# Kernel optimization log

Hardware: AMD Instinct MI355X
Metric: run time of the kernel (lower is better)

The kernel has to match this reference:

```python
import jax, jax.numpy as jnp
import numpy as np

B, S, DIN, DOUT = 4, 2048, 4096, 4096
W_SCALE = 64.0   # makes round(weight*scale) produce non-trivial int8 values
X_SCALE = 16.0   # input_scale so x*scale truncates to non-zero int32 values


def setup_inputs() -> dict:
    key = jax.random.key(0)
    k1, k2, k3 = jax.random.split(key, 3)
    # kaiming_uniform fan_in: bound = sqrt(6/fan_in)
    bound = float(np.sqrt(6.0 / DIN))
    weight = jax.random.uniform(k1, (DOUT, DIN), jnp.float32, -bound, bound)
    x = jax.random.normal(k2, (B, S, DIN), jnp.float32)
    bias = jax.random.normal(k3, (DOUT,), jnp.float32) * 0.01
    weight_scale = jnp.full((DOUT,), W_SCALE, jnp.float32)
    input_scale = jnp.full((1,), X_SCALE, jnp.float32)
    return {"x": x, "weight": weight, "bias": bias,
            "weight_scale": weight_scale, "input_scale": input_scale}


def reference(x, weight, bias, weight_scale, input_scale):
    # x = x * input_scale (pre-scale path of forward)
    xs = x * input_scale
    # fake-quant weights: round to int8 with wraparound, like torch .to(int8)
    w_int = jnp.round(weight * weight_scale[:, None]).astype(jnp.int8)
    # x.to(torch.int32): truncation toward zero
    x_int = xs.astype(jnp.int32)
    # F.linear on the integer-valued tensors (computed in f32: values are exact ints)
    acc = jnp.einsum('bsd,od->bso', x_int.astype(jnp.float32),
                     w_int.astype(jnp.float32))
    acc = acc + bias  # bias added inside linear
    # dequant: divide by per-channel weight_scale and the scalar input_scale
    out = acc / (weight_scale * input_scale)
    return out
```

## Files before the change

kernel.cpp:

```cpp
#include <hip/hip_runtime.h>

#define GM 8192
#define GN 4096
#define GK 4096

#define BM 256
#define BN 256
#define BK 64
#define NTILE (GK / BK)
#define ABYTES (BM * BK)
#define TILE_LDS (BM * BK + BN * BK)

using int4v = __attribute__((ext_vector_type(4))) int;

__global__ __launch_bounds__(256) void quant_xw_k(
    const float4* __restrict__ x, unsigned int* __restrict__ xq,
    const float4* __restrict__ w, unsigned int* __restrict__ wq,
    const float* __restrict__ wscale, const float* __restrict__ iscale,
    int n4x, int n4tot) {
    const float xs = *iscale;
    const int stride = gridDim.x * blockDim.x;
    for (int i = blockIdx.x * blockDim.x + threadIdx.x; i < n4tot; i += stride) {
        if (i < n4x) {
            float4 v = x[i];
            int q0 = (int)(v.x * xs);
            int q1 = (int)(v.y * xs);
            int q2 = (int)(v.z * xs);
            int q3 = (int)(v.w * xs);
            xq[i] = (unsigned int)(q0 & 0xff)
                  | ((unsigned int)(q1 & 0xff) << 8)
                  | ((unsigned int)(q2 & 0xff) << 16)
                  | ((unsigned int)(q3 & 0xff) << 24);
        } else {
            int j = i - n4x;
            float s = wscale[j >> 10];
            float4 v = w[j];
            int q0 = (int)rintf(v.x * s);
            int q1 = (int)rintf(v.y * s);
            int q2 = (int)rintf(v.z * s);
            int q3 = (int)rintf(v.w * s);
            wq[j] = (unsigned int)(q0 & 0xff)
                  | ((unsigned int)(q1 & 0xff) << 8)
                  | ((unsigned int)(q2 & 0xff) << 16)
                  | ((unsigned int)(q3 & 0xff) << 24);
        }
    }
}

__global__ __launch_bounds__(512, 2) void qlinear_gemm_i8(
    const signed char* __restrict__ Aq,
    const signed char* __restrict__ Bq,
    const float* __restrict__ bias,
    const float* __restrict__ wscale,
    const float* __restrict__ iscale,
    float* __restrict__ C) {
    __shared__ signed char smem[3 * TILE_LDS];

    const int tid  = threadIdx.x;
    const int wave = tid >> 6;
    const int lane = tid & 63;
    const int m0 = blockIdx.x * BM;
    const int n0 = blockIdx.y * BN;
    const int wm = (wave >> 2) * 128;
    const int wn = (wave & 3) * 64;

    int4v acc[8][4];
#pragma unroll
    for (int i = 0; i < 8; ++i)
#pragma unroll
        for (int j = 0; j < 4; ++j)
            acc[i][j] = int4v{0, 0, 0, 0};

    const int kc = ((tid & 3) ^ ((tid >> 3) & 3)) * 16;
    const signed char* gA = Aq + (size_t)(m0 + (tid >> 2)) * GK + kc;
    const signed char* gB = Bq + (size_t)(n0 + (tid >> 2)) * GK + kc;
    const int dst = tid * 16;

    const int pos = (((lane >> 4) ^ ((lane >> 1) & 3))) * 16;
    const int fAo = (wm + (lane & 15)) * BK + pos;
    const int fBo = ABYTES + (wn + (lane & 15)) * BK + pos;

#define GLL16(g, l)                                                     \
    __builtin_amdgcn_global_load_lds(                                   \
        (__attribute__((address_space(1))) void*)(void*)(g),            \
        (__attribute__((address_space(3))) void*)(void*)(l), 16, 0, 0)

#define STAGE_A(kb, soff)                                               \
    do {                                                                \
        GLL16(gA + (kb), smem + (soff) + dst);                          \
        GLL16(gA + (size_t)128 * GK + (kb), smem + (soff) + 8192 + dst);\
    } while (0)
#define STAGE_B(kb, soff)                                               \
    do {                                                                \
        GLL16(gB + (kb), smem + (soff) + ABYTES + dst);                 \
        GLL16(gB + (size_t)128 * GK + (kb),                             \
              smem + (soff) + ABYTES + 8192 + dst);                     \
    } while (0)

    STAGE_A(0, 0);
    STAGE_B(0, 0);
    STAGE_A(BK, TILE_LDS);
    STAGE_B(BK, TILE_LDS);
    asm volatile("s_waitcnt vmcnt(4)" ::: "memory");
    __builtin_amdgcn_s_barrier();
    __builtin_amdgcn_sched_barrier(0);

    int bc = 0;
    int bn2 = TILE_LDS;
    int bs = 2 * TILE_LDS;
    int kst = 2 * BK;
    for (int t = 0; t < NTILE; ++t) {
        const signed char* fA = smem + bc + fAo;
        const signed char* fB = smem + bc + fBo;
        int4v aF[4], bF[4], aG[4];

#pragma unroll
        for (int i = 0; i < 4; ++i)
            aF[i] = *(const int4v*)(fA + i * 1024);
#pragma unroll
        for (int j = 0; j < 4; ++j)
            bF[j] = *(const int4v*)(fB + j * 1024);
        STAGE_A(kst, bs);
        __builtin_amdgcn_s_barrier();
        asm volatile("s_waitcnt lgkmcnt(0)" ::: "memory");
        __builtin_amdgcn_sched_barrier(0);
        __builtin_amdgcn_s_setprio(1);
#pragma unroll
        for (int i = 0; i < 4; ++i)
#pragma unroll
            for (int j = 0; j < 4; ++j)
                acc[i][j] = __builtin_amdgcn_mfma_i32_16x16x64_i8(
                    aF[i], bF[j], acc[i][j], 0, 0, 0);
        __builtin_amdgcn_s_setprio(0);
        __builtin_amdgcn_s_barrier();
        __builtin_amdgcn_sched_barrier(0);

#pragma unroll
        for (int i = 0; i < 4; ++i)
            aG[i] = *(const int4v*)(fA + (i + 4) * 1024);
        STAGE_B(kst, bs);
        __builtin_amdgcn_s_barrier();
        asm volatile("s_waitcnt lgkmcnt(0)" ::: "memory");
        __builtin_amdgcn_sched_barrier(0);
        __builtin_amdgcn_s_setprio(1);
#pragma unroll
        for (int i = 0; i < 4; ++i)
#pragma unroll
            for (int j = 0; j < 4; ++j)
                acc[i + 4][j] = __builtin_amdgcn_mfma_i32_16x16x64_i8(
                    aG[i], bF[j], acc[i + 4][j], 0, 0, 0);
        __builtin_amdgcn_s_setprio(0);
        asm volatile("s_waitcnt vmcnt(4)" ::: "memory");
        __builtin_amdgcn_s_barrier();
        __builtin_amdgcn_sched_barrier(0);

        int tmp = bc; bc = bn2; bn2 = bs; bs = tmp;
        kst += BK; if (kst >= GK) kst = 0;
    }

    const float isc = *iscale;
#pragma unroll
    for (int ni = 0; ni < 4; ++ni) {
        const int col = n0 + wn + ni * 16 + (lane & 15);
        const float bs_ = bias[col];
        const float inv = 1.0f / (wscale[col] * isc);
#pragma unroll
        for (int mi = 0; mi < 8; ++mi) {
            const int row0 = m0 + wm + mi * 16 + (lane >> 4) * 4;
#pragma unroll
            for (int r = 0; r < 4; ++r) {
                C[(size_t)(row0 + r) * GN + col] =
                    ((float)acc[mi][ni][r] + bs_) * inv;
            }
        }
    }
#undef STAGE_A
#undef STAGE_B
#undef GLL16
}

extern "C" void kernel_launch(void* const* d_in, const int* in_sizes, int n_in,
                              void* d_out, int out_size, void* d_ws, size_t ws_size,
                              hipStream_t stream) {
    const float* x      = (const float*)d_in[0];
    const float* w      = (const float*)d_in[1];
    const float* bias   = (const float*)d_in[2];
    const float* wscale = (const float*)d_in[3];
    const float* iscale = (const float*)d_in[4];
    float* out = (float*)d_out;

    signed char* xq = (signed char*)d_ws;
    signed char* wq = xq + (size_t)GM * GK;

    const int n4x = GM * GK / 4;
    const int n4w = GN * GK / 4;
    quant_xw_k<<<3072, 256, 0, stream>>>((const float4*)x, (unsigned int*)xq,
                                         (const float4*)w, (unsigned int*)wq,
                                         wscale, iscale, n4x, n4x + n4w);

    dim3 grid(GM / BM, GN / BN);
    qlinear_gemm_i8<<<grid, 512, 0, stream>>>(xq, wq, bias, wscale, iscale, out);
}
```

Measured before the change: 399.6 us.

## Shrink GEMM block tile to 128x256 and simplify per-tile pipeline

Halves the M dimension of the int8 GEMM block tile, so each wave holds a 4x4 MFMA accumulator grid instead of 8x4. The K-loop is flattened into a single phase: it issues the whole next-stage async copy up front, then does one fragment load and one MFMA batch, with one barrier per tile. The aim is to cut register pressure and barrier count and to raise the occupancy hint to four blocks. The cost is lower data reuse per block, so there is more global and LDS traffic per FLOP. LDS use per block may also keep the achieved occupancy below the hint.

```diff
diff --git a/kernel.cpp b/kernel.cpp
--- a/kernel.cpp
+++ b/kernel.cpp
@@ -4,12 +4,12 @@
 #define GN 4096
 #define GK 4096
 
-#define BM 256
+#define BM 128
 #define BN 256
 #define BK 64
 #define NTILE (GK / BK)
 #define ABYTES (BM * BK)
-#define TILE_LDS (BM * BK + BN * BK)
+#define TILE_LDS (ABYTES + BN * BK)
 
 using int4v = __attribute__((ext_vector_type(4))) int;
 
@@ -47,7 +47,7 @@
     }
 }
 
-__global__ __launch_bounds__(512, 2) void qlinear_gemm_i8(
+__global__ __launch_bounds__(512, 4) void qlinear_gemm_i8(
     const signed char* __restrict__ Aq,
     const signed char* __restrict__ Bq,
     const float* __restrict__ bias,
@@ -61,12 +61,12 @@
     const int lane = tid & 63;
     const int m0 = blockIdx.x * BM;
     const int n0 = blockIdx.y * BN;
-    const int wm = (wave >> 2) * 128;
+    const int wm = (wave >> 2) * 64;
     const int wn = (wave & 3) * 64;
 
-    int4v acc[8][4];
+    int4v acc[4][4];
 #pragma unroll
-    for (int i = 0; i < 8; ++i)
+    for (int i = 0; i < 4; ++i)
 #pragma unroll
         for (int j = 0; j < 4; ++j)
             acc[i][j] = int4v{0, 0, 0, 0};
@@ -85,23 +85,17 @@
         (__attribute__((address_space(1))) void*)(void*)(g),            \
         (__attribute__((address_space(3))) void*)(void*)(l), 16, 0, 0)
 
-#define STAGE_A(kb, soff)                                               \
+#define STAGE(kb, soff)                                                 \
     do {                                                                \
         GLL16(gA + (kb), smem + (soff) + dst);                          \
-        GLL16(gA + (size_t)128 * GK + (kb), smem + (soff) + 8192 + dst);\
-    } while (0)
-#define STAGE_B(kb, soff)                                               \
-    do {                                                                \
         GLL16(gB + (kb), smem + (soff) + ABYTES + dst);                 \
         GLL16(gB + (size_t)128 * GK + (kb),                             \
               smem + (soff) + ABYTES + 8192 + dst);                     \
     } while (0)
 
-    STAGE_A(0, 0);
-    STAGE_B(0, 0);
-    STAGE_A(BK, TILE_LDS);
-    STAGE_B(BK, TILE_LDS);
-    asm volatile("s_waitcnt vmcnt(4)" ::: "memory");
+    STAGE(0, 0);
+    STAGE(BK, TILE_LDS);
+    asm volatile("s_waitcnt vmcnt(3)" ::: "memory");
     __builtin_amdgcn_s_barrier();
     __builtin_amdgcn_sched_barrier(0);
 
@@ -110,47 +104,29 @@
     int bs = 2 * TILE_LDS;
     int kst = 2 * BK;
     for (int t = 0; t < NTILE; ++t) {
+        STAGE(kst, bs);
+        __builtin_amdgcn_sched_barrier(0);
+
         const signed char* fA = smem + bc + fAo;
         const signed char* fB = smem + bc + fBo;
-        int4v aF[4], bF[4], aG[4];
-
+        int4v a[4], b[4];
 #pragma unroll
         for (int i = 0; i < 4; ++i)
-            aF[i] = *(const int4v*)(fA + i * 1024);
+            a[i] = *(const int4v*)(fA + i * 1024);
 #pragma unroll
         for (int j = 0; j < 4; ++j)
-            bF[j] = *(const int4v*)(fB + j * 1024);
-        STAGE_A(kst, bs);
-        __builtin_amdgcn_s_barrier();
-        asm volatile("s_waitcnt lgkmcnt(0)" ::: "memory");
-        __builtin_amdgcn_sched_barrier(0);
+            b[j] = *(const int4v*)(fB + j * 1024);
+
         __builtin_amdgcn_s_setprio(1);
 #pragma unroll
-        for (int i = 0; i < 4; ++i)
+        for (int mi = 0; mi < 4; ++mi)
 #pragma unroll
-            for (int j = 0; j < 4; ++j)
-                acc[i][j] = __builtin_amdgcn_mfma_i32_16x16x64_i8(
-                    aF[i], bF[j], acc[i][j], 0, 0, 0);
+            for (int ni = 0; ni < 4; ++ni)
+                acc[mi][ni] = __builtin_amdgcn_mfma_i32_16x16x64_i8(
+                    a[mi], b[ni], acc[mi][ni], 0, 0, 0);
         __builtin_amdgcn_s_setprio(0);
-        __builtin_amdgcn_s_barrier();
-        __builtin_amdgcn_sched_barrier(0);
 
-#pragma unroll
-        for (int i = 0; i < 4; ++i)
-            aG[i] = *(const int4v*)(fA + (i + 4) * 1024);
-        STAGE_B(kst, bs);
-        __builtin_amdgcn_s_barrier();
-        asm volatile("s_waitcnt lgkmcnt(0)" ::: "memory");
-        __builtin_amdgcn_sched_barrier(0);
-        __builtin_amdgcn_s_setprio(1);
-#pragma unroll
-        for (int i = 0; i < 4; ++i)
-#pragma unroll
-            for (int j = 0; j < 4; ++j)
-                acc[i + 4][j] = __builtin_amdgcn_mfma_i32_16x16x64_i8(
-                    aG[i], bF[j], acc[i + 4][j], 0, 0, 0);
-        __builtin_amdgcn_s_setprio(0);
-        asm volatile("s_waitcnt vmcnt(4)" ::: "memory");
+        asm volatile("s_waitcnt vmcnt(3)" ::: "memory");
         __builtin_amdgcn_s_barrier();
         __builtin_amdgcn_sched_barrier(0);
 
@@ -165,7 +141,7 @@
         const float bs_ = bias[col];
         const float inv = 1.0f / (wscale[col] * isc);
 #pragma unroll
-        for (int mi = 0; mi < 8; ++mi) {
+        for (int mi = 0; mi < 4; ++mi) {
             const int row0 = m0 + wm + mi * 16 + (lane >> 4) * 4;
 #pragma unroll
             for (int r = 0; r < 4; ++r) {
@@ -174,8 +150,7 @@
             }
         }
     }
-#undef STAGE_A
-#undef STAGE_B
+#undef STAGE
 #undef GLL16
 }
 
```

Result: no change. 404.3 us (+1.2%).
